# Kernel tuning notes

Hardware: AMD Instinct MI355X
Metric: run time of the kernel (lower is better)

The kernel has to match this reference:

```python
import jax, jax.numpy as jnp
import numpy as np

H = 512
S = 65  # 64 board cells + appended constant 1


def _heads(y, wk, wq, wv):
    # y: [H, S]; wk/wq/wv: [3, H, H] -> atts: [3, S, H]
    def one(wk_i, wq_i, wv_i):
        k = wk_i @ y            # [H, S]
        q = wq_i @ y            # [H, S]
        v = wv_i @ y            # [H, S]
        sm = jax.nn.softmax(k.T @ q, axis=1)  # [S, S], softmax over dim=1
        return sm @ v.T         # [S, H]
    return jax.vmap(one)(wk, wq, wv)


def setup_inputs() -> dict:
    key = jax.random.key(0)
    ks = jax.random.split(key, 10)
    r = lambda k, s: jax.random.normal(k, s, dtype=jnp.float32)
    return {
        "inputs": r(ks[0], (1, 64)),
        "embedding": r(ks[1], (H, S)),
        "wq": r(ks[2], (3, 3, H, H)),
        "wk": r(ks[3], (3, 3, H, H)),
        "wv": r(ks[4], (3, 3, H, H)),
        "linear1": r(ks[5], (3 * H, H)),
        "linear2": r(ks[6], (3 * H, H)),
        "linear3": r(ks[7], (3 * H, 2 * H)),
        "linear4": r(ks[8], (2 * H, H)),
        "linear5": r(ks[9], (H, 64)),
    }


def reference(inputs, embedding, wq, wk, wv, linear1, linear2, linear3, linear4, linear5):
    x = jnp.concatenate([inputs[0], jnp.ones((1,), inputs.dtype)])  # [S]
    y = embedding * x  # [H, S] (broadcast over rows)

    # Layer 1 (3 heads)
    a1 = _heads(y, wk[0], wq[0], wv[0])  # [3, S, H]
    y = jax.nn.relu(jnp.concatenate([a1[0], a1[1], a1[2]], axis=1) @ linear1).T  # [H, S]

    # Layer 2 -- NOTE: original code cats att11, att12, att23 (a bug we preserve)
    a2 = _heads(y, wk[1], wq[1], wv[1])
    y = jax.nn.relu(jnp.concatenate([a1[0], a1[1], a2[2]], axis=1) @ linear2).T  # [H, S]

    # Layer 3 -- NOTE: original code cats att11, att12, att33 (preserved)
    a3 = _heads(y, wk[2], wq[2], wv[2])
    y = jax.nn.relu(jnp.concatenate([a1[0], a1[1], a3[2]], axis=1) @ linear3)[64]  # [2H]

    # dropout p=0.1 -> identity in eval mode
    y = jnp.tanh(y @ linear4)  # [H]
    score = y @ linear5        # [64]
    return score[None, :]      # [1, 64]
```

## Files before the change

### kernel.cpp

```cpp
#include <hip/hip_runtime.h>
#include <hip/hip_bf16.h>
#include <math.h>

#define H 512
#define S 65
#define SP 80
#define HS (H * S)
#define PHS (H * SP)
#define KS3 24
#define KS4 16


__global__ void scale_embed_kernel(const float* __restrict__ inp,
                                   const float* __restrict__ emb,
                                   float* __restrict__ yT) {
    int i = blockIdx.x * blockDim.x + threadIdx.x;
    if (i < PHS) {
        int s = i / H;
        int h = i % H;
        float v = 0.f;
        if (s < S) {
            float x = (s == 64) ? 1.0f : inp[s];
            v = emb[h * S + s] * x;
        }
        yT[i] = v;
    }
}

__device__ __forceinline__ void mac4(float4& c, float ax, float ay, float az,
                                     float aw, const float4& w0, const float4& w1,
                                     const float4& w2, const float4& w3) {
    c.x = fmaf(ax, w0.x, c.x); c.y = fmaf(ax, w0.y, c.y);
    c.z = fmaf(ax, w0.z, c.z); c.w = fmaf(ax, w0.w, c.w);
    c.x = fmaf(ay, w1.x, c.x); c.y = fmaf(ay, w1.y, c.y);
    c.z = fmaf(ay, w1.z, c.z); c.w = fmaf(ay, w1.w, c.w);
    c.x = fmaf(az, w2.x, c.x); c.y = fmaf(az, w2.y, c.y);
    c.z = fmaf(az, w2.z, c.z); c.w = fmaf(az, w2.w, c.w);
    c.x = fmaf(aw, w3.x, c.x); c.y = fmaf(aw, w3.y, c.y);
    c.z = fmaf(aw, w3.z, c.z); c.w = fmaf(aw, w3.w, c.w);
}

template <int KSPLIT>
__global__ void __launch_bounds__(256, 1)
kqv_gemm_tiled(const float* __restrict__ wq,
               const float* __restrict__ wk,
               const float* __restrict__ wv,
               int mat0,
               const float* __restrict__ yT,
               float* __restrict__ part) {
    int slot  = blockIdx.z;
    int which = blockIdx.y;
    int mat = mat0 + slot;
    const float* W = (which == 0 ? wk : (which == 1 ? wq : wv)) + (size_t)mat * H * H;

    int n0   = (blockIdx.x & 15) * 32;
    int kidx = blockIdx.x >> 4;
    const int NCH = 8 / KSPLIT;

    __shared__ float Wt[64 * 32];
    __shared__ float As[SP * 68];

    int t  = threadIdx.x;
    int nq = t & 7;
    int g  = t >> 3;
    bool r2 = (g < 16);

    float4 acc0 = {0,0,0,0}, acc1 = {0,0,0,0}, acc2 = {0,0,0,0};

    for (int ch = 0; ch < NCH; ++ch) {
        int kc0 = (kidx * NCH + ch) * 64;
#pragma unroll
        for (int c = 0; c < 2; ++c) {
            int f = c * 256 + t;
            int wn  = f >> 4;
            int kf4 = f & 15;
            float4 w4 = *(const float4*)(W + (size_t)(n0 + wn) * H + kc0 + 4 * kf4);
            int sw = ((wn >> 2) ^ (kf4 & 7));
            int base = (4 * kf4) * 32 + 4 * sw + (wn & 3);
            Wt[base     ] = w4.x;
            Wt[base + 32] = w4.y;
            Wt[base + 64] = w4.z;
            Wt[base + 96] = w4.w;
        }
#pragma unroll
        for (int c = 0; c < 5; ++c) {
            int f = c * 256 + t;
            int as  = f >> 4;
            int kf4 = f & 15;
            *(float4*)(&As[as * 68 + 4 * kf4]) =
                *(const float4*)(yT + (size_t)as * H + kc0 + 4 * kf4);
        }
        __syncthreads();

#pragma unroll
        for (int k4 = 0; k4 < 16; ++k4) {
            int swc = 4 * (nq ^ (k4 & 7));
            float4 w0 = *(const float4*)(&Wt[(4 * k4 + 0) * 32 + swc]);
            float4 w1 = *(const float4*)(&Wt[(4 * k4 + 1) * 32 + swc]);
            float4 w2 = *(const float4*)(&Wt[(4 * k4 + 2) * 32 + swc]);
            float4 w3 = *(const float4*)(&Wt[(4 * k4 + 3) * 32 + swc]);
            {
                float4 a = *(const float4*)(&As[g * 68 + 4 * k4]);
                mac4(acc0, a.x, a.y, a.z, a.w, w0, w1, w2, w3);
            }
            {
                float4 a = *(const float4*)(&As[(g + 32) * 68 + 4 * k4]);
                mac4(acc1, a.x, a.y, a.z, a.w, w0, w1, w2, w3);
            }
            if (r2) {
                float4 a = *(const float4*)(&As[(g + 64) * 68 + 4 * k4]);
                mac4(acc2, a.x, a.y, a.z, a.w, w0, w1, w2, w3);
            }
        }
        __syncthreads();
    }

    float* P = part + (size_t)((slot * 3 + which) * KSPLIT + kidx) * PHS;
    *(float4*)(P + (size_t)g * H + n0 + 4 * nq) = acc0;
    *(float4*)(P + (size_t)(g + 32) * H + n0 + 4 * nq) = acc1;
    if (r2) *(float4*)(P + (size_t)(g + 64) * H + n0 + 4 * nq) = acc2;
}

template <int NS>
__device__ __forceinline__ float score_part(const float* __restrict__ Q,
                                            const float* __restrict__ ka,
                                            int b, int t) {
    const float4* q0 = (const float4*)(Q + (size_t)b * H) + t * 32;
    const float4* q1 = (const float4*)(Q + PHS + (size_t)b * H) + t * 32;
    const float4* kl = (const float4*)ka + t * 32;
    float4 c0 = {0,0,0,0}, c1 = {0,0,0,0};
#pragma unroll
    for (int u = 0; u < 32; u += 2) {
        float4 qa = q0[u], qc = q0[u + 1];
        float4 k0 = kl[u], k1 = kl[u + 1];
        if (NS == 2) {
            float4 qb = q1[u], qd = q1[u + 1];
            qa.x += qb.x; qa.y += qb.y; qa.z += qb.z; qa.w += qb.w;
            qc.x += qd.x; qc.y += qd.y; qc.z += qd.z; qc.w += qd.w;
        }
        c0.x = fmaf(k0.x, qa.x, c0.x);
        c0.y = fmaf(k0.y, qa.y, c0.y);
        c0.z = fmaf(k0.z, qa.z, c0.z);
        c0.w = fmaf(k0.w, qa.w, c0.w);
        c1.x = fmaf(k1.x, qc.x, c1.x);
        c1.y = fmaf(k1.y, qc.y, c1.y);
        c1.z = fmaf(k1.z, qc.z, c1.z);
        c1.w = fmaf(k1.w, qc.w, c1.w);
    }
    return ((c0.x + c0.y) + (c0.z + c0.w)) + ((c1.x + c1.y) + (c1.z + c1.w));
}

template <int NS>
__global__ void attn_kernel(const float* __restrict__ kqvp,
                            float* __restrict__ att) {
    int a = blockIdx.x;
    int slot = blockIdx.y;
    int tid = threadIdx.x;

    const float* base = kqvp + (size_t)slot * 3 * NS * PHS;
    const float* K0 = base;
    const float* Q0 = base + (size_t)NS * PHS;
    const float* V0 = base + (size_t)2 * NS * PHS;
    const float* K1 = K0 + PHS;
    const float* V1 = V0 + PHS;
    float* ao = att + (size_t)slot * PHS + (size_t)a * H;

    __shared__ float ka[H];
    __shared__ float sp[4 * 65];
    __shared__ float smv[S];
    __shared__ float p[S];

    if (NS == 2) {
        ka[tid]       = K0[(size_t)a * H + tid]       + K1[(size_t)a * H + tid];
        ka[tid + 256] = K0[(size_t)a * H + tid + 256] + K1[(size_t)a * H + tid + 256];
    } else {
        ka[tid]       = K0[(size_t)a * H + tid];
        ka[tid + 256] = K0[(size_t)a * H + tid + 256];
    }
    __syncthreads();

    {
        int b = tid & 63;
        int t = tid >> 6;
        sp[t * 65 + b] = score_part<NS>(Q0, ka, b, t);
        if (tid < 4) sp[tid * 65 + 64] = score_part<NS>(Q0, ka, 64, tid);
    }
    __syncthreads();

    if (tid < S) {
        smv[tid] = (sp[tid] + sp[65 + tid]) + (sp[130 + tid] + sp[195 + tid]);
    }
    __syncthreads();

    float maxv = -INFINITY;
    for (int i = 0; i < S; ++i) maxv = fmaxf(maxv, smv[i]);
    float sum = 0.0f;
    for (int i = 0; i < S; ++i) sum += expf(smv[i] - maxv);
    float inv = 1.0f / sum;
    if (tid < S) p[tid] = expf(smv[tid] - maxv) * inv;
    __syncthreads();

#pragma unroll
    for (int rep = 0; rep < 2; ++rep) {
        int hh = tid + rep * 256;
        float a0 = 0.f, a1 = 0.f;
#pragma unroll 4
        for (int b = 0; b < 64; b += 2) {
            float v0 = V0[(size_t)(b    ) * H + hh];
            float v1 = V0[(size_t)(b + 1) * H + hh];
            if (NS == 2) {
                v0 += V1[(size_t)(b    ) * H + hh];
                v1 += V1[(size_t)(b + 1) * H + hh];
            }
            a0 = fmaf(p[b    ], v0, a0);
            a1 = fmaf(p[b + 1], v1, a1);
        }
        {
            float v0 = V0[(size_t)64 * H + hh];
            if (NS == 2) v0 += V1[(size_t)64 * H + hh];
            a0 = fmaf(p[64], v0, a0);
        }
        ao[hh] = a0 + a1;
    }
}

__device__ __forceinline__ void lin4row_dev(const float* __restrict__ att,
                                            int col0,
                                            const float* __restrict__ L,
                                            float* __restrict__ dst,
                                            int s0, int tid) {
    __shared__ float Ar[4 * 256];
    __shared__ float4 red[4 * 128];

    {
        int rr = tid >> 6;
        int cc = tid & 63;
        *(float4*)(&Ar[rr * 256 + cc * 4]) =
            *(const float4*)(att + (size_t)(s0 + rr) * H + col0 + cc * 4);
    }
    __syncthreads();

    int h4 = (tid & 127) * 4;
    int jh = tid >> 7;
    const float* Lj = L + (size_t)(jh * 128) * H + h4;
    const float* A0 = Ar + jh * 128;

    float4 c0 = {0,0,0,0}, c1 = {0,0,0,0}, c2 = {0,0,0,0}, c3 = {0,0,0,0};
#pragma unroll 8
    for (int j = 0; j < 128; ++j) {
        float4 L4 = *(const float4*)(Lj + (size_t)j * H);
        float a0 = A0[j], a1 = A0[256 + j], a2 = A0[512 + j], a3 = A0[768 + j];
        c0.x = fmaf(a0, L4.x, c0.x); c0.y = fmaf(a0, L4.y, c0.y);
        c0.z = fmaf(a0, L4.z, c0.z); c0.w = fmaf(a0, L4.w, c0.w);
        c1.x = fmaf(a1, L4.x, c1.x); c1.y = fmaf(a1, L4.y, c1.y);
        c1.z = fmaf(a1, L4.z, c1.z); c1.w = fmaf(a1, L4.w, c1.w);
        c2.x = fmaf(a2, L4.x, c2.x); c2.y = fmaf(a2, L4.y, c2.y);
        c2.z = fmaf(a2, L4.z, c2.z); c2.w = fmaf(a2, L4.w, c2.w);
        c3.x = fmaf(a3, L4.x, c3.x); c3.y = fmaf(a3, L4.y, c3.y);
        c3.z = fmaf(a3, L4.z, c3.z); c3.w = fmaf(a3, L4.w, c3.w);
    }

    if (jh == 1) {
        int x = tid & 127;
        red[x] = c0; red[128 + x] = c1; red[256 + x] = c2; red[384 + x] = c3;
    }
    __syncthreads();
    if (jh == 0) {
        float4 r0 = red[tid], r1 = red[128 + tid], r2 = red[256 + tid], r3 = red[384 + tid];
        c0.x += r0.x; c0.y += r0.y; c0.z += r0.z; c0.w += r0.w;
        c1.x += r1.x; c1.y += r1.y; c1.z += r1.z; c1.w += r1.w;
        c2.x += r2.x; c2.y += r2.y; c2.z += r2.z; c2.w += r2.w;
        c3.x += r3.x; c3.y += r3.y; c3.z += r3.z; c3.w += r3.w;
        *(float4*)(dst + (size_t)(s0 + 0) * H + h4) = c0;
        *(float4*)(dst + (size_t)(s0 + 1) * H + h4) = c1;
        *(float4*)(dst + (size_t)(s0 + 2) * H + h4) = c2;
        *(float4*)(dst + (size_t)(s0 + 3) * H + h4) = c3;
    }
}

__global__ void mega_lin_kernel(const float* __restrict__ att1,
                                const float* __restrict__ lin1,
                                const float* __restrict__ lin2,
                                const float* __restrict__ lin3,
                                float* __restrict__ plin1,
                                float* __restrict__ plin2,
                                float* __restrict__ tpart) {
    int bx = blockIdx.x;
    int tid = threadIdx.x;

    if (bx < 170) {
        int seg = bx / 17;
        int p   = bx % 17;
        const float* att;
        const float* L;
        float* dst;
        if (seg < 6) {
            att = att1 + (size_t)(seg >> 1) * PHS;
            L   = lin1 + (size_t)(seg * 256) * H;
            dst = plin1 + (size_t)seg * PHS;
        } else {
            int s2 = seg - 6;
            att = att1 + (size_t)(s2 >> 1) * PHS;
            L   = lin2 + (size_t)(s2 * 256) * H;
            dst = plin2 + (size_t)s2 * PHS;
        }
        lin4row_dev(att, (seg & 1) * 256, L, dst, p * 4, tid);
    } else {
        int idx = bx - 170;
        int j2 = (idx & 3) * 256 + tid;
        int ks = idx >> 2;
        const float* row = att1 + (size_t)(ks >> 3) * PHS + (size_t)64 * H;
        int j0 = (ks & 7) * 64;
        int jbase = ks * 64;
        float a0 = 0.f, a1 = 0.f, a2 = 0.f, a3 = 0.f;
        for (int j = 0; j < 64; j += 4) {
            a0 = fmaf(row[j0 + j + 0], lin3[(size_t)(jbase + j + 0) * 1024 + j2], a0);
            a1 = fmaf(row[j0 + j + 1], lin3[(size_t)(jbase + j + 1) * 1024 + j2], a1);
            a2 = fmaf(row[j0 + j + 2], lin3[(size_t)(jbase + j + 2) * 1024 + j2], a2);
            a3 = fmaf(row[j0 + j + 3], lin3[(size_t)(jbase + j + 3) * 1024 + j2], a3);
        }
        tpart[ks * 1024 + j2] = (a0 + a1) + (a2 + a3);
    }
}

__global__ void combine6_relu_kernel(const float* __restrict__ part,
                                     float* __restrict__ yT) {
    int i = blockIdx.x * 256 + threadIdx.x;
    float s = 0.f;
#pragma unroll
    for (int p = 0; p < 6; ++p) s += part[(size_t)p * PHS + i];
    yT[i] = fmaxf(s, 0.0f);
}

__global__ void lin2c_combine_kernel(const float* __restrict__ att2,
                                     const float* __restrict__ lin2,
                                     const float* __restrict__ plin2,
                                     float* __restrict__ yT) {
    int i = blockIdx.x * 256 + threadIdx.x;
    int s = i / H;
    int h = i % H;
    const float* row = att2 + (size_t)s * H;
    const float* L4 = lin2 + (size_t)1024 * H + h;
    const float* L5 = lin2 + (size_t)1280 * H + h;

    float a0 = 0.f, a1 = 0.f, a2 = 0.f, a3 = 0.f;
    for (int j = 0; j < 256; j += 4) {
        a0 = fmaf(row[j + 0], L4[(size_t)(j + 0) * H], a0);
        a1 = fmaf(row[j + 1], L4[(size_t)(j + 1) * H], a1);
        a2 = fmaf(row[j + 2], L4[(size_t)(j + 2) * H], a2);
        a3 = fmaf(row[j + 3], L4[(size_t)(j + 3) * H], a3);
    }
    for (int j = 0; j < 256; j += 4) {
        a0 = fmaf(row[256 + j + 0], L5[(size_t)(j + 0) * H], a0);
        a1 = fmaf(row[256 + j + 1], L5[(size_t)(j + 1) * H], a1);
        a2 = fmaf(row[256 + j + 2], L5[(size_t)(j + 2) * H], a2);
        a3 = fmaf(row[256 + j + 3], L5[(size_t)(j + 3) * H], a3);
    }
    float tot = (a0 + a1) + (a2 + a3)
              + plin2[i] + plin2[PHS + i] + plin2[2 * PHS + i] + plin2[3 * PHS + i];
    yT[i] = fmaxf(tot, 0.0f);
}

__global__ void attn3_lin3c_kernel(const float* __restrict__ kqvp,
                                   const float* __restrict__ lin3,
                                   float* __restrict__ tpart) {
    int tid = threadIdx.x;
    int ks  = 16 + blockIdx.y;
    int j2  = blockIdx.x * 256 + tid;
    int j0  = (ks & 7) * 64;

    const float* K0 = kqvp;
    const float* K1 = kqvp + PHS;
    const float* Q0 = kqvp + 2 * (size_t)PHS;
    const float* V0 = kqvp + 4 * (size_t)PHS;
    const float* V1 = kqvp + 5 * (size_t)PHS;

    __shared__ float ka[H];
    __shared__ float sp[4 * 65];
    __shared__ float smv[S];
    __shared__ float p[S];
    __shared__ float att_s[64];

    ka[tid]       = K0[(size_t)64 * H + tid]       + K1[(size_t)64 * H + tid];
    ka[tid + 256] = K0[(size_t)64 * H + tid + 256] + K1[(size_t)64 * H + tid + 256];
    __syncthreads();

    {
        int b = tid & 63;
        int t = tid >> 6;
        sp[t * 65 + b] = score_part<2>(Q0, ka, b, t);
        if (tid < 4) sp[tid * 65 + 64] = score_part<2>(Q0, ka, 64, tid);
    }
    __syncthreads();

    if (tid < S) {
        smv[tid] = (sp[tid] + sp[65 + tid]) + (sp[130 + tid] + sp[195 + tid]);
    }
    __syncthreads();

    float maxv = -INFINITY;
    for (int i = 0; i < S; ++i) maxv = fmaxf(maxv, smv[i]);
    float sum = 0.0f;
    for (int i = 0; i < S; ++i) sum += expf(smv[i] - maxv);
    float inv = 1.0f / sum;
    if (tid < S) p[tid] = expf(smv[tid] - maxv) * inv;
    __syncthreads();

    if (tid < 64) {
        int hh = j0 + tid;
        float a0 = 0.f, a1 = 0.f;
#pragma unroll 4
        for (int b = 0; b < 64; b += 2) {
            a0 = fmaf(p[b    ], V0[(size_t)(b    ) * H + hh] + V1[(size_t)(b    ) * H + hh], a0);
            a1 = fmaf(p[b + 1], V0[(size_t)(b + 1) * H + hh] + V1[(size_t)(b + 1) * H + hh], a1);
        }
        a0 = fmaf(p[64], V0[(size_t)64 * H + hh] + V1[(size_t)64 * H + hh], a0);
        att_s[tid] = a0 + a1;
    }
    __syncthreads();

    int jbase = ks * 64;
    float a0 = 0.f, a1 = 0.f, a2 = 0.f, a3 = 0.f;
    for (int j = 0; j < 64; j += 4) {
        a0 = fmaf(att_s[j + 0], lin3[(size_t)(jbase + j + 0) * 1024 + j2], a0);
        a1 = fmaf(att_s[j + 1], lin3[(size_t)(jbase + j + 1) * 1024 + j2], a1);
        a2 = fmaf(att_s[j + 2], lin3[(size_t)(jbase + j + 2) * 1024 + j2], a2);
        a3 = fmaf(att_s[j + 3], lin3[(size_t)(jbase + j + 3) * 1024 + j2], a3);
    }
    tpart[ks * 1024 + j2] = (a0 + a1) + (a2 + a3);
}

__global__ void lin4_partial_kernel(const float* __restrict__ tpart,
                                    const float* __restrict__ lin4,
                                    float* __restrict__ upart) {
    __shared__ float tl[64];
    int hh = blockIdx.x * 256 + threadIdx.x;
    int ks = blockIdx.y;
    int j2base = ks * 64;

    if (threadIdx.x < 64) {
        int j2 = j2base + threadIdx.x;
        float s = 0.f;
#pragma unroll
        for (int p = 0; p < KS3; ++p) s += tpart[p * 1024 + j2];
        tl[threadIdx.x] = fmaxf(s, 0.f);
    }
    __syncthreads();

    float a0 = 0.f, a1 = 0.f, a2 = 0.f, a3 = 0.f;
    for (int j = 0; j < 64; j += 4) {
        a0 = fmaf(tl[j + 0], lin4[(size_t)(j2base + j + 0) * H + hh], a0);
        a1 = fmaf(tl[j + 1], lin4[(size_t)(j2base + j + 1) * H + hh], a1);
        a2 = fmaf(tl[j + 2], lin4[(size_t)(j2base + j + 2) * H + hh], a2);
        a3 = fmaf(tl[j + 3], lin4[(size_t)(j2base + j + 3) * H + hh], a3);
    }
    upart[ks * H + hh] = (a0 + a1) + (a2 + a3);
}

__global__ void final_out_kernel(const float* __restrict__ upart,
                                 const float* __restrict__ lin5,
                                 float* __restrict__ out) {
    __shared__ float u[H];
    __shared__ float pr[8][64];
    int tid = threadIdx.x;

    {
        float s = 0.f;
#pragma unroll
        for (int p = 0; p < KS4; ++p) s += upart[p * H + tid];
        u[tid] = tanhf(s);
    }
    __syncthreads();

    int o  = tid & 63;
    int sl = tid >> 6;
    float acc = 0.f;
    int h0 = sl * 64;
#pragma unroll 8
    for (int j = 0; j < 64; ++j) {
        acc = fmaf(u[h0 + j], lin5[(h0 + j) * 64 + o], acc);
    }
    pr[sl][o] = acc;
    __syncthreads();

    if (tid < 64) {
        float s = 0.f;
#pragma unroll
        for (int p = 0; p < 8; ++p) s += pr[p][tid];
        out[tid] = s;
    }
}

extern "C" void kernel_launch(void* const* d_in, const int* in_sizes, int n_in,
                              void* d_out, int out_size, void* d_ws, size_t ws_size,
                              hipStream_t stream) {
    const float* inputs  = (const float*)d_in[0];
    const float* emb     = (const float*)d_in[1];
    const float* wq      = (const float*)d_in[2];
    const float* wk      = (const float*)d_in[3];
    const float* wv      = (const float*)d_in[4];
    const float* linear1 = (const float*)d_in[5];
    const float* linear2 = (const float*)d_in[6];
    const float* linear3 = (const float*)d_in[7];
    const float* linear4 = (const float*)d_in[8];
    const float* linear5 = (const float*)d_in[9];
    float* out = (float*)d_out;

    float* ws    = (float*)d_ws;
    float* y     = ws;
    float* kqvp  = y     + PHS;
    float* att1  = kqvp  + 9 * PHS;
    float* att2  = att1  + 3 * PHS;
    float* plin1 = att2  + PHS;
    float* plin2 = plin1 + 6 * PHS;
    float* tpart = plin2 + 4 * PHS;
    float* upart = tpart + KS3 * 1024;

    const int nb  = HS / 256;
    const int nbp = PHS / 256;

    scale_embed_kernel<<<nbp, 256, 0, stream>>>(inputs, emb, y);

    kqv_gemm_tiled<1><<<dim3(16, 3, 3), 256, 0, stream>>>(wq, wk, wv, 0, y, kqvp);
    attn_kernel<1><<<dim3(S, 3), 256, 0, stream>>>(kqvp, att1);
    mega_lin_kernel<<<234, 256, 0, stream>>>(att1, linear1, linear2, linear3,
                                             plin1, plin2, tpart);
    combine6_relu_kernel<<<nb, 256, 0, stream>>>(plin1, y);

    kqv_gemm_tiled<2><<<dim3(32, 3, 1), 256, 0, stream>>>(wq, wk, wv, 5, y, kqvp);
    attn_kernel<2><<<dim3(S, 1), 256, 0, stream>>>(kqvp, att2);
    lin2c_combine_kernel<<<nb, 256, 0, stream>>>(att2, linear2, plin2, y);

    kqv_gemm_tiled<2><<<dim3(32, 3, 1), 256, 0, stream>>>(wq, wk, wv, 8, y, kqvp);
    attn3_lin3c_kernel<<<dim3(4, 8), 256, 0, stream>>>(kqvp, linear3, tpart);

    lin4_partial_kernel<<<dim3(2, KS4), 256, 0, stream>>>(tpart, linear4, upart);
    final_out_kernel<<<1, 512, 0, stream>>>(upart, linear5, out);
}
```

Measured before the change: 259.4 us.

## Replace split-K partial buffers with atomic accumulation and fuse combine kernels

```diff
diff --git a/kernel.cpp b/kernel.cpp
--- a/kernel.cpp
+++ b/kernel.cpp
@@ -7,14 +7,16 @@
 #define SP 80
 #define HS (H * S)
 #define PHS (H * SP)
-#define KS3 24
-#define KS4 16
-
-
-__global__ void scale_embed_kernel(const float* __restrict__ inp,
-                                   const float* __restrict__ emb,
-                                   float* __restrict__ yT) {
-    int i = blockIdx.x * blockDim.x + threadIdx.x;
+
+
+__global__ void scale_embed_zero_kernel(const float* __restrict__ inp,
+                                        const float* __restrict__ emb,
+                                        float* __restrict__ yT,
+                                        float* __restrict__ y2acc,
+                                        float* __restrict__ pacc2,
+                                        float* __restrict__ tacc,
+                                        float* __restrict__ uacc) {
+    int i = blockIdx.x * 256 + threadIdx.x;
     if (i < PHS) {
         int s = i / H;
         int h = i % H;
@@ -24,6 +26,14 @@
             v = emb[h * S + s] * x;
         }
         yT[i] = v;
+        y2acc[i] = 0.f;
+        pacc2[i] = 0.f;
+    }
+    if (blockIdx.x == 0) {
+        int t = threadIdx.x;
+        tacc[t] = 0.f; tacc[256 + t] = 0.f; tacc[512 + t] = 0.f; tacc[768 + t] = 0.f;
+        uacc[t & 511] = 0.f;
+        uacc[256 + t] = 0.f;
     }
 }
 
@@ -40,13 +50,13 @@
     c.z = fmaf(aw, w3.z, c.z); c.w = fmaf(aw, w3.w, c.w);
 }
 
-template <int KSPLIT>
+template <int KSPLIT, int RELU>
 __global__ void __launch_bounds__(256, 1)
 kqv_gemm_tiled(const float* __restrict__ wq,
                const float* __restrict__ wk,
                const float* __restrict__ wv,
                int mat0,
-               const float* __restrict__ yT,
+               const float* __restrict__ src,
                float* __restrict__ part) {
     int slot  = blockIdx.z;
     int which = blockIdx.y;
@@ -87,8 +97,12 @@
             int f = c * 256 + t;
             int as  = f >> 4;
             int kf4 = f & 15;
-            *(float4*)(&As[as * 68 + 4 * kf4]) =
-                *(const float4*)(yT + (size_t)as * H + kc0 + 4 * kf4);
+            float4 v = *(const float4*)(src + (size_t)as * H + kc0 + 4 * kf4);
+            if (RELU) {
+                v.x = fmaxf(v.x, 0.f); v.y = fmaxf(v.y, 0.f);
+                v.z = fmaxf(v.z, 0.f); v.w = fmaxf(v.w, 0.f);
+            }
+            *(float4*)(&As[as * 68 + 4 * kf4]) = v;
         }
         __syncthreads();
 
@@ -125,19 +139,22 @@
 __device__ __forceinline__ float score_part(const float* __restrict__ Q,
                                             const float* __restrict__ ka,
                                             int b, int t) {
-    const float4* q0 = (const float4*)(Q + (size_t)b * H) + t * 32;
-    const float4* q1 = (const float4*)(Q + PHS + (size_t)b * H) + t * 32;
+    const float4* q[NS];
+#pragma unroll
+    for (int n = 0; n < NS; ++n)
+        q[n] = (const float4*)(Q + (size_t)n * PHS + (size_t)b * H) + t * 32;
     const float4* kl = (const float4*)ka + t * 32;
     float4 c0 = {0,0,0,0}, c1 = {0,0,0,0};
 #pragma unroll
     for (int u = 0; u < 32; u += 2) {
-        float4 qa = q0[u], qc = q0[u + 1];
-        float4 k0 = kl[u], k1 = kl[u + 1];
-        if (NS == 2) {
-            float4 qb = q1[u], qd = q1[u + 1];
+        float4 qa = q[0][u], qc = q[0][u + 1];
+#pragma unroll
+        for (int n = 1; n < NS; ++n) {
+            float4 qb = q[n][u], qd = q[n][u + 1];
             qa.x += qb.x; qa.y += qb.y; qa.z += qb.z; qa.w += qb.w;
             qc.x += qd.x; qc.y += qd.y; qc.z += qd.z; qc.w += qd.w;
         }
+        float4 k0 = kl[u], k1 = kl[u + 1];
         c0.x = fmaf(k0.x, qa.x, c0.x);
         c0.y = fmaf(k0.y, qa.y, c0.y);
         c0.z = fmaf(k0.z, qa.z, c0.z);
@@ -151,39 +168,27 @@
 }
 
 template <int NS>
-__global__ void attn_kernel(const float* __restrict__ kqvp,
-                            float* __restrict__ att) {
-    int a = blockIdx.x;
-    int slot = blockIdx.y;
-    int tid = threadIdx.x;
-
-    const float* base = kqvp + (size_t)slot * 3 * NS * PHS;
-    const float* K0 = base;
-    const float* Q0 = base + (size_t)NS * PHS;
-    const float* V0 = base + (size_t)2 * NS * PHS;
-    const float* K1 = K0 + PHS;
-    const float* V1 = V0 + PHS;
-    float* ao = att + (size_t)slot * PHS + (size_t)a * H;
-
-    __shared__ float ka[H];
-    __shared__ float sp[4 * 65];
-    __shared__ float smv[S];
-    __shared__ float p[S];
-
-    if (NS == 2) {
-        ka[tid]       = K0[(size_t)a * H + tid]       + K1[(size_t)a * H + tid];
-        ka[tid + 256] = K0[(size_t)a * H + tid + 256] + K1[(size_t)a * H + tid + 256];
-    } else {
-        ka[tid]       = K0[(size_t)a * H + tid];
-        ka[tid + 256] = K0[(size_t)a * H + tid + 256];
-    }
+__device__ __forceinline__ void attn_body(const float* __restrict__ K,
+                                          const float* __restrict__ Q,
+                                          int a, int tid,
+                                          float* __restrict__ ka,
+                                          float* __restrict__ sp,
+                                          float* __restrict__ smv,
+                                          float* __restrict__ p) {
+    float k0 = 0.f, k1 = 0.f;
+#pragma unroll
+    for (int n = 0; n < NS; ++n) {
+        k0 += K[(size_t)n * PHS + (size_t)a * H + tid];
+        k1 += K[(size_t)n * PHS + (size_t)a * H + tid + 256];
+    }
+    ka[tid] = k0; ka[tid + 256] = k1;
     __syncthreads();
 
     {
         int b = tid & 63;
         int t = tid >> 6;
-        sp[t * 65 + b] = score_part<NS>(Q0, ka, b, t);
-        if (tid < 4) sp[tid * 65 + 64] = score_part<NS>(Q0, ka, 64, tid);
+        sp[t * 65 + b] = score_part<NS>(Q, ka, b, t);
+        if (tid < 4) sp[tid * 65 + 64] = score_part<NS>(Q, ka, 64, tid);
     }
     __syncthreads();
 
@@ -199,6 +204,26 @@
     float inv = 1.0f / sum;
     if (tid < S) p[tid] = expf(smv[tid] - maxv) * inv;
     __syncthreads();
+}
+
+__global__ void attn1_kernel(const float* __restrict__ kqvp,
+                             float* __restrict__ att) {
+    int a = blockIdx.x;
+    int slot = blockIdx.y;
+    int tid = threadIdx.x;
+
+    const float* base = kqvp + (size_t)slot * 6 * PHS;
+    const float* K = base;
+    const float* Q = base + 2 * (size_t)PHS;
+    const float* V = base + 4 * (size_t)PHS;
+    float* ao = att + (size_t)slot * PHS + (size_t)a * H;
+
+    __shared__ float ka[H];
+    __shared__ float sp[4 * 65];
+    __shared__ float smv[S];
+    __shared__ float p[S];
+
+    attn_body<2>(K, Q, a, tid, ka, sp, smv, p);
 
 #pragma unroll
     for (int rep = 0; rep < 2; ++rep) {
@@ -206,29 +231,21 @@
         float a0 = 0.f, a1 = 0.f;
 #pragma unroll 4
         for (int b = 0; b < 64; b += 2) {
-            float v0 = V0[(size_t)(b    ) * H + hh];
-            float v1 = V0[(size_t)(b + 1) * H + hh];
-            if (NS == 2) {
-                v0 += V1[(size_t)(b    ) * H + hh];
-                v1 += V1[(size_t)(b + 1) * H + hh];
-            }
+            float v0 = V[(size_t)(b    ) * H + hh] + V[PHS + (size_t)(b    ) * H + hh];
+            float v1 = V[(size_t)(b + 1) * H + hh] + V[PHS + (size_t)(b + 1) * H + hh];
             a0 = fmaf(p[b    ], v0, a0);
             a1 = fmaf(p[b + 1], v1, a1);
         }
-        {
-            float v0 = V0[(size_t)64 * H + hh];
-            if (NS == 2) v0 += V1[(size_t)64 * H + hh];
-            a0 = fmaf(p[64], v0, a0);
-        }
+        a0 = fmaf(p[64], V[(size_t)64 * H + hh] + V[PHS + (size_t)64 * H + hh], a0);
         ao[hh] = a0 + a1;
     }
 }
 
-__device__ __forceinline__ void lin4row_dev(const float* __restrict__ att,
-                                            int col0,
-                                            const float* __restrict__ L,
-                                            float* __restrict__ dst,
-                                            int s0, int tid) {
+__device__ __forceinline__ void lin4row_atomic_dev(const float* __restrict__ att,
+                                                   int col0,
+                                                   const float* __restrict__ L,
+                                                   float* __restrict__ dst,
+                                                   int s0, int tid) {
     __shared__ float Ar[4 * 256];
     __shared__ float4 red[4 * 128];
 
@@ -271,10 +288,18 @@
         c1.x += r1.x; c1.y += r1.y; c1.z += r1.z; c1.w += r1.w;
         c2.x += r2.x; c2.y += r2.y; c2.z += r2.z; c2.w += r2.w;
         c3.x += r3.x; c3.y += r3.y; c3.z += r3.z; c3.w += r3.w;
-        *(float4*)(dst + (size_t)(s0 + 0) * H + h4) = c0;
-        *(float4*)(dst + (size_t)(s0 + 1) * H + h4) = c1;
-        *(float4*)(dst + (size_t)(s0 + 2) * H + h4) = c2;
-        *(float4*)(dst + (size_t)(s0 + 3) * H + h4) = c3;
+        float* d0 = dst + (size_t)(s0 + 0) * H + h4;
+        float* d1 = dst + (size_t)(s0 + 1) * H + h4;
+        float* d2 = dst + (size_t)(s0 + 2) * H + h4;
+        float* d3 = dst + (size_t)(s0 + 3) * H + h4;
+        atomicAdd(d0 + 0, c0.x); atomicAdd(d0 + 1, c0.y);
+        atomicAdd(d0 + 2, c0.z); atomicAdd(d0 + 3, c0.w);
+        atomicAdd(d1 + 0, c1.x); atomicAdd(d1 + 1, c1.y);
+        atomicAdd(d1 + 2, c1.z); atomicAdd(d1 + 3, c1.w);
+        atomicAdd(d2 + 0, c2.x); atomicAdd(d2 + 1, c2.y);
+        atomicAdd(d2 + 2, c2.z); atomicAdd(d2 + 3, c2.w);
+        atomicAdd(d3 + 0, c3.x); atomicAdd(d3 + 1, c3.y);
+        atomicAdd(d3 + 2, c3.z); atomicAdd(d3 + 3, c3.w);
     }
 }
 
@@ -282,29 +307,29 @@
                                 const float* __restrict__ lin1,
                                 const float* __restrict__ lin2,
                                 const float* __restrict__ lin3,
-                                float* __restrict__ plin1,
-                                float* __restrict__ plin2,
-                                float* __restrict__ tpart) {
+                                float* __restrict__ y2acc,
+                                float* __restrict__ pacc2,
+                                float* __restrict__ tacc) {
     int bx = blockIdx.x;
     int tid = threadIdx.x;
 
     if (bx < 170) {
         int seg = bx / 17;
-        int p   = bx % 17;
+        int pnum = bx % 17;
         const float* att;
         const float* L;
         float* dst;
         if (seg < 6) {
             att = att1 + (size_t)(seg >> 1) * PHS;
             L   = lin1 + (size_t)(seg * 256) * H;
-            dst = plin1 + (size_t)seg * PHS;
+            dst = y2acc;
         } else {
             int s2 = seg - 6;
             att = att1 + (size_t)(s2 >> 1) * PHS;
             L   = lin2 + (size_t)(s2 * 256) * H;
-            dst = plin2 + (size_t)s2 * PHS;
-        }
-        lin4row_dev(att, (seg & 1) * 256, L, dst, p * 4, tid);
+            dst = pacc2;
+        }
+        lin4row_atomic_dev(att, (seg & 1) * 256, L, dst, pnum * 4, tid);
     } else {
         int idx = bx - 170;
         int j2 = (idx & 3) * 256 + tid;
@@ -319,61 +344,94 @@
             a2 = fmaf(row[j0 + j + 2], lin3[(size_t)(jbase + j + 2) * 1024 + j2], a2);
             a3 = fmaf(row[j0 + j + 3], lin3[(size_t)(jbase + j + 3) * 1024 + j2], a3);
         }
-        tpart[ks * 1024 + j2] = (a0 + a1) + (a2 + a3);
-    }
-}
-
-__global__ void combine6_relu_kernel(const float* __restrict__ part,
-                                     float* __restrict__ yT) {
-    int i = blockIdx.x * 256 + threadIdx.x;
-    float s = 0.f;
-#pragma unroll
-    for (int p = 0; p < 6; ++p) s += part[(size_t)p * PHS + i];
-    yT[i] = fmaxf(s, 0.0f);
-}
-
-__global__ void lin2c_combine_kernel(const float* __restrict__ att2,
-                                     const float* __restrict__ lin2,
-                                     const float* __restrict__ plin2,
-                                     float* __restrict__ yT) {
-    int i = blockIdx.x * 256 + threadIdx.x;
-    int s = i / H;
-    int h = i % H;
-    const float* row = att2 + (size_t)s * H;
-    const float* L4 = lin2 + (size_t)1024 * H + h;
-    const float* L5 = lin2 + (size_t)1280 * H + h;
-
-    float a0 = 0.f, a1 = 0.f, a2 = 0.f, a3 = 0.f;
-    for (int j = 0; j < 256; j += 4) {
-        a0 = fmaf(row[j + 0], L4[(size_t)(j + 0) * H], a0);
-        a1 = fmaf(row[j + 1], L4[(size_t)(j + 1) * H], a1);
-        a2 = fmaf(row[j + 2], L4[(size_t)(j + 2) * H], a2);
-        a3 = fmaf(row[j + 3], L4[(size_t)(j + 3) * H], a3);
-    }
-    for (int j = 0; j < 256; j += 4) {
-        a0 = fmaf(row[256 + j + 0], L5[(size_t)(j + 0) * H], a0);
-        a1 = fmaf(row[256 + j + 1], L5[(size_t)(j + 1) * H], a1);
-        a2 = fmaf(row[256 + j + 2], L5[(size_t)(j + 2) * H], a2);
-        a3 = fmaf(row[256 + j + 3], L5[(size_t)(j + 3) * H], a3);
-    }
-    float tot = (a0 + a1) + (a2 + a3)
-              + plin2[i] + plin2[PHS + i] + plin2[2 * PHS + i] + plin2[3 * PHS + i];
-    yT[i] = fmaxf(tot, 0.0f);
+        atomicAdd(&tacc[j2], (a0 + a1) + (a2 + a3));
+    }
+}
+
+__global__ void attn2_lin2_kernel(const float* __restrict__ kqvp,
+                                  const float* __restrict__ lin2,
+                                  const float* __restrict__ pacc2,
+                                  float* __restrict__ y3) {
+    int a = blockIdx.x;
+    int tid = threadIdx.x;
+
+    const float* K = kqvp;
+    const float* Q = kqvp + 4 * (size_t)PHS;
+    const float* V = kqvp + 8 * (size_t)PHS;
+
+    __shared__ float ka[H];
+    __shared__ float sp[4 * 65];
+    __shared__ float smv[S];
+    __shared__ float p[S];
+    __shared__ float arow[H];
+    __shared__ float4 red[128];
+
+    attn_body<4>(K, Q, a, tid, ka, sp, smv, p);
+
+#pragma unroll
+    for (int rep = 0; rep < 2; ++rep) {
+        int hh = tid + rep * 256;
+        float a0 = 0.f, a1 = 0.f;
+#pragma unroll 4
+        for (int b = 0; b < 64; b += 2) {
+            float v0 = 0.f, v1 = 0.f;
+#pragma unroll
+            for (int n = 0; n < 4; ++n) {
+                v0 += V[(size_t)n * PHS + (size_t)(b    ) * H + hh];
+                v1 += V[(size_t)n * PHS + (size_t)(b + 1) * H + hh];
+            }
+            a0 = fmaf(p[b    ], v0, a0);
+            a1 = fmaf(p[b + 1], v1, a1);
+        }
+        {
+            float v0 = 0.f;
+#pragma unroll
+            for (int n = 0; n < 4; ++n) v0 += V[(size_t)n * PHS + (size_t)64 * H + hh];
+            a0 = fmaf(p[64], v0, a0);
+        }
+        arow[hh] = a0 + a1;
+    }
+    __syncthreads();
+
+    int h4 = (tid & 127) * 4;
+    int jh = tid >> 7;
+    const float* Lj = lin2 + (size_t)(1024 + jh * 256) * H + h4;
+    const float* A0 = arow + jh * 256;
+
+    float4 c = {0,0,0,0};
+#pragma unroll 8
+    for (int j = 0; j < 256; ++j) {
+        float4 L4 = *(const float4*)(Lj + (size_t)j * H);
+        float av = A0[j];
+        c.x = fmaf(av, L4.x, c.x);
+        c.y = fmaf(av, L4.y, c.y);
+        c.z = fmaf(av, L4.z, c.z);
+        c.w = fmaf(av, L4.w, c.w);
+    }
+    if (jh == 1) red[tid & 127] = c;
+    __syncthreads();
+    if (jh == 0) {
+        float4 r = red[tid];
+        float4 pa = *(const float4*)(pacc2 + (size_t)a * H + h4);
+        c.x = fmaxf(c.x + r.x + pa.x, 0.f);
+        c.y = fmaxf(c.y + r.y + pa.y, 0.f);
+        c.z = fmaxf(c.z + r.z + pa.z, 0.f);
+        c.w = fmaxf(c.w + r.w + pa.w, 0.f);
+        *(float4*)(y3 + (size_t)a * H + h4) = c;
+    }
 }
 
 __global__ void attn3_lin3c_kernel(const float* __restrict__ kqvp,
                                    const float* __restrict__ lin3,
-                                   float* __restrict__ tpart) {
+                                   float* __restrict__ tacc) {
     int tid = threadIdx.x;
     int ks  = 16 + blockIdx.y;
     int j2  = blockIdx.x * 256 + tid;
     int j0  = (ks & 7) * 64;
 
-    const float* K0 = kqvp;
-    const float* K1 = kqvp + PHS;
-    const float* Q0 = kqvp + 2 * (size_t)PHS;
-    const float* V0 = kqvp + 4 * (size_t)PHS;
-    const float* V1 = kqvp + 5 * (size_t)PHS;
+    const float* K = kqvp;
+    const float* Q = kqvp + 4 * (size_t)PHS;
+    const float* V = kqvp + 8 * (size_t)PHS;
 
     __shared__ float ka[H];
     __shared__ float sp[4 * 65];
@@ -381,40 +439,28 @@
     __shared__ float p[S];
     __shared__ float att_s[64];
 
-    ka[tid]       = K0[(size_t)64 * H + tid]       + K1[(size_t)64 * H + tid];
-    ka[tid + 256] = K0[(size_t)64 * H + tid + 256] + K1[(size_t)64 * H + tid + 256];
-    __syncthreads();
-
-    {
-        int b = tid & 63;
-        int t = tid >> 6;
-        sp[t * 65 + b] = score_part<2>(Q0, ka, b, t);
-        if (tid < 4) sp[tid * 65 + 64] = score_part<2>(Q0, ka, 64, tid);
-    }
-    __syncthreads();
-
-    if (tid < S) {
-        smv[tid] = (sp[tid] + sp[65 + tid]) + (sp[130 + tid] + sp[195 + tid]);
-    }
-    __syncthreads();
-
-    float maxv = -INFINITY;
-    for (int i = 0; i < S; ++i) maxv = fmaxf(maxv, smv[i]);
-    float sum = 0.0f;
-    for (int i = 0; i < S; ++i) sum += expf(smv[i] - maxv);
-    float inv = 1.0f / sum;
-    if (tid < S) p[tid] = expf(smv[tid] - maxv) * inv;
-    __syncthreads();
+    attn_body<4>(K, Q, 64, tid, ka, sp, smv, p);
 
     if (tid < 64) {
         int hh = j0 + tid;
         float a0 = 0.f, a1 = 0.f;
 #pragma unroll 4
         for (int b = 0; b < 64; b += 2) {
-            a0 = fmaf(p[b    ], V0[(size_t)(b    ) * H + hh] + V1[(size_t)(b    ) * H + hh], a0);
-            a1 = fmaf(p[b + 1], V0[(size_t)(b + 1) * H + hh] + V1[(size_t)(b + 1) * H + hh], a1);
-        }
-        a0 = fmaf(p[64], V0[(size_t)64 * H + hh] + V1[(size_t)64 * H + hh], a0);
+            float v0 = 0.f, v1 = 0.f;
+#pragma unroll
+            for (int n = 0; n < 4; ++n) {
+                v0 += V[(size_t)n * PHS + (size_t)(b    ) * H + hh];
+                v1 += V[(size_t)n * PHS + (size_t)(b + 1) * H + hh];
+            }
+            a0 = fmaf(p[b    ], v0, a0);
+            a1 = fmaf(p[b + 1], v1, a1);
+        }
+        {
+            float v0 = 0.f;
+#pragma unroll
+            for (int n = 0; n < 4; ++n) v0 += V[(size_t)n * PHS + (size_t)64 * H + hh];
+            a0 = fmaf(p[64], v0, a0);
+        }
         att_s[tid] = a0 + a1;
     }
     __syncthreads();
@@ -427,23 +473,19 @@
         a2 = fmaf(att_s[j + 2], lin3[(size_t)(jbase + j + 2) * 1024 + j2], a2);
         a3 = fmaf(att_s[j + 3], lin3[(size_t)(jbase + j + 3) * 1024 + j2], a3);
     }
-    tpart[ks * 1024 + j2] = (a0 + a1) + (a2 + a3);
-}
-
-__global__ void lin4_partial_kernel(const float* __restrict__ tpart,
-                                    const float* __restrict__ lin4,
-                                    float* __restrict__ upart) {
+    atomicAdd(&tacc[j2], (a0 + a1) + (a2 + a3));
+}
+
+__global__ void lin4_kernel(const float* __restrict__ tacc,
+                            const float* __restrict__ lin4,
+                            float* __restrict__ uacc) {
     __shared__ float tl[64];
     int hh = blockIdx.x * 256 + threadIdx.x;
     int ks = blockIdx.y;
     int j2base = ks * 64;
 
     if (threadIdx.x < 64) {
-        int j2 = j2base + threadIdx.x;
-        float s = 0.f;
-#pragma unroll
-        for (int p = 0; p < KS3; ++p) s += tpart[p * 1024 + j2];
-        tl[threadIdx.x] = fmaxf(s, 0.f);
+        tl[threadIdx.x] = fmaxf(tacc[j2base + threadIdx.x], 0.f);
     }
     __syncthreads();
 
@@ -454,22 +496,17 @@
         a2 = fmaf(tl[j + 2], lin4[(size_t)(j2base + j + 2) * H + hh], a2);
         a3 = fmaf(tl[j + 3], lin4[(size_t)(j2base + j + 3) * H + hh], a3);
     }
-    upart[ks * H + hh] = (a0 + a1) + (a2 + a3);
-}
-
-__global__ void final_out_kernel(const float* __restrict__ upart,
+    atomicAdd(&uacc[hh], (a0 + a1) + (a2 + a3));
+}
+
+__global__ void final_out_kernel(const float* __restrict__ uacc,
                                  const float* __restrict__ lin5,
                                  float* __restrict__ out) {
     __shared__ float u[H];
     __shared__ float pr[8][64];
     int tid = threadIdx.x;
 
-    {
-        float s = 0.f;
-#pragma unroll
-        for (int p = 0; p < KS4; ++p) s += upart[p * H + tid];
-        u[tid] = tanhf(s);
-    }
+    u[tid] = tanhf(uacc[tid]);
     __syncthreads();
 
     int o  = tid & 63;
@@ -507,33 +544,31 @@
     float* out = (float*)d_out;
 
     float* ws    = (float*)d_ws;
-    float* y     = ws;
-    float* kqvp  = y     + PHS;
-    float* att1  = kqvp  + 9 * PHS;
-    float* att2  = att1  + 3 * PHS;
-    float* plin1 = att2  + PHS;
-    float* plin2 = plin1 + 6 * PHS;
-    float* tpart = plin2 + 4 * PHS;
-    float* upart = tpart + KS3 * 1024;
-
-    const int nb  = HS / 256;
+    float* y1    = ws;
+    float* kqvp  = y1    + PHS;
+    float* att1  = kqvp  + 18 * PHS;
+    float* y2acc = att1  + 3 * PHS;
+    float* pacc2 = y2acc + PHS;
+    float* y3    = pacc2 + PHS;
+    float* tacc  = y3    + PHS;
+    float* uacc  = tacc  + 1024;
+
     const int nbp = PHS / 256;
 
-    scale_embed_kernel<<<nbp, 256, 0, stream>>>(inputs, emb, y);
-
-    kqv_gemm_tiled<1><<<dim3(16, 3, 3), 256, 0, stream>>>(wq, wk, wv, 0, y, kqvp);
-    attn_kernel<1><<<dim3(S, 3), 256, 0, stream>>>(kqvp, att1);
+    scale_embed_zero_kernel<<<nbp, 256, 0, stream>>>(inputs, emb, y1,
+                                                     y2acc, pacc2, tacc, uacc);
+
+    kqv_gemm_tiled<2, 0><<<dim3(32, 3, 3), 256, 0, stream>>>(wq, wk, wv, 0, y1, kqvp);
+    attn1_kernel<<<dim3(S, 3), 256, 0, stream>>>(kqvp, att1);
     mega_lin_kernel<<<234, 256, 0, stream>>>(att1, linear1, linear2, linear3,
-                                             plin1, plin2, tpart);
-    combine6_relu_kernel<<<nb, 256, 0, stream>>>(plin1, y);
-
-    kqv_gemm_tiled<2><<<dim3(32, 3, 1), 256, 0, stream>>>(wq, wk, wv, 5, y, kqvp);
-    attn_kernel<2><<<dim3(S, 1), 256, 0, stream>>>(kqvp, att2);
-    lin2c_combine_kernel<<<nb, 256, 0, stream>>>(att2, linear2, plin2, y);
-
-    kqv_gemm_tiled<2><<<dim3(32, 3, 1), 256, 0, stream>>>(wq, wk, wv, 8, y, kqvp);
-    attn3_lin3c_kernel<<<dim3(4, 8), 256, 0, stream>>>(kqvp, linear3, tpart);
-
-    lin4_partial_kernel<<<dim3(2, KS4), 256, 0, stream>>>(tpart, linear4, upart);
-    final_out_kernel<<<1, 512, 0, stream>>>(upart, linear5, out);
-}
+                                             y2acc, pacc2, tacc);
+
+    kqv_gemm_tiled<4, 1><<<dim3(64, 3, 1), 256, 0, stream>>>(wq, wk, wv, 5, y2acc, kqvp);
+    attn2_lin2_kernel<<<S, 256, 0, stream>>>(kqvp, linear2, pacc2, y3);
+
+    kqv_gemm_tiled<4, 0><<<dim3(64, 3, 1), 256, 0, stream>>>(wq, wk, wv, 8, y3, kqvp);
+    attn3_lin3c_kernel<<<dim3(4, 8), 256, 0, stream>>>(kqvp, linear3, tacc);
+
+    lin4_kernel<<<dim3(2, 16), 256, 0, stream>>>(tacc, linear4, uacc);
+    final_out_kernel<<<1, 512, 0, stream>>>(uacc, linear5, out);
+}
```

New measurement: 308.9 us. 19.1% more time.
